# Optimization experiments

Measured on AMD Instinct MI355X. Metric: run time of the kernel, lower is better.

## Reference

```python
import jax, jax.numpy as jnp
import numpy as np

D_MODEL = 1024
NUM_HEADS = 16
ROPE_BASE = 10000.0


def _rope_sincos(T, head_dim, dtype):
    # angles[t, i] = t / base**(2i/head_dim), i in [0, head_dim//2)
    pos = jnp.arange(T, dtype=jnp.float32)[:, None]              # [T, 1]
    inv_freq = 1.0 / (ROPE_BASE ** (jnp.arange(0, head_dim, 2, dtype=jnp.float32) / head_dim))
    angles = pos * inv_freq                                       # [T, half]
    sin = jnp.sin(angles).astype(dtype)[None, :, None, :]         # [1, T, 1, half]
    cos = jnp.cos(angles).astype(dtype)[None, :, None, :]
    return sin, cos


def _apply_rope(x, sin, cos):
    # x: [B, T, H, head_dim]; deinterleave even/odd lanes, rotate, concat halves
    x1, x2 = x[..., ::2], x[..., 1::2]                            # [B, T, H, half] each
    return jnp.concatenate([x1 * cos - x2 * sin, x1 * sin + x2 * cos], axis=-1)


def setup_inputs() -> dict:
    key = jax.random.key(0)
    ks = jax.random.split(key, 5)
    B, T, D = 2, 2048, D_MODEL
    s = 0.02
    return {
        "x": jax.random.normal(ks[0], (B, T, D), dtype=jnp.float32),
        "w_qkv": jax.random.normal(ks[1], (3 * D, D), dtype=jnp.float32) * s,
        "b_qkv": jnp.zeros((3 * D,), dtype=jnp.float32),
        "w_out": jax.random.normal(ks[2], (D, D), dtype=jnp.float32) * s,
        "b_out": jnp.zeros((D,), dtype=jnp.float32),
    }


def reference(x, w_qkv, b_qkv, w_out, b_out):
    B, T, D = x.shape
    H = NUM_HEADS
    hd = D // H
    scale = hd ** -0.5

    qkv = (x @ w_qkv.T + b_qkv).reshape(B, T, 3, H, hd)
    q, k, v = qkv[:, :, 0], qkv[:, :, 1], qkv[:, :, 2]            # [B, T, H, hd]

    sin, cos = _rope_sincos(T, hd, x.dtype)
    q = _apply_rope(q, sin, cos)
    k = _apply_rope(k, sin, cos)

    scores = jnp.einsum("bthd,bshd->bhts", q, k) * scale          # [B, H, T, T]
    weights = jax.nn.softmax(scores, axis=-1)
    out = jnp.einsum("bhts,bshd->bthd", weights, v)               # [B, T, H, hd]
    out = out.reshape(B, T, D)
    return out @ w_out.T + b_out
```

## Files before the change

kernel.cpp:

```cpp
#include <hip/hip_runtime.h>
#include <cstdint>
#include <cstddef>

typedef __attribute__((ext_vector_type(8))) short short8;
typedef __attribute__((ext_vector_type(8))) __bf16 bf16x8;
typedef __attribute__((ext_vector_type(4))) float f32x4;
typedef __attribute__((ext_vector_type(16))) float f32x16;
typedef __attribute__((ext_vector_type(4))) unsigned int uint32x4;

#define LOG2E 1.44269504088896340736f

__device__ __forceinline__ unsigned short f2bf(float f) {
    unsigned int u = __builtin_bit_cast(unsigned int, f);
    u += 0x7fffu + ((u >> 16) & 1u);
    return (unsigned short)(u >> 16);
}

__device__ __forceinline__ f32x4 zero4() {
    f32x4 z; z.x = 0.f; z.y = 0.f; z.z = 0.f; z.w = 0.f; return z;
}
__device__ __forceinline__ f32x16 zero16() {
    f32x16 z;
    #pragma unroll
    for (int i = 0; i < 16; ++i) z[i] = 0.f;
    return z;
}

__device__ __forceinline__ f32x4 mfma16(short8 a, short8 b, f32x4 c) {
    return __builtin_amdgcn_mfma_f32_16x16x32_bf16(
        __builtin_bit_cast(bf16x8, a), __builtin_bit_cast(bf16x8, b), c, 0, 0, 0);
}
__device__ __forceinline__ f32x16 mfma32(short8 a, short8 b, f32x16 c) {
    return __builtin_amdgcn_mfma_f32_32x32x16_bf16(
        __builtin_bit_cast(bf16x8, a), __builtin_bit_cast(bf16x8, b), c, 0, 0, 0);
}

__device__ __forceinline__ unsigned int cvt_pk_bf16(float lo, float hi) {
    unsigned int r;
    asm("v_cvt_pk_bf16_f32 %0, %1, %2" : "=v"(r) : "v"(lo), "v"(hi));
    return r;
}

__device__ __forceinline__ uint2 permswap(unsigned x, unsigned y) {
#if __has_builtin(__builtin_amdgcn_permlane32_swap)
    auto r = __builtin_amdgcn_permlane32_swap(x, y, false, false);
    return make_uint2(r[0], r[1]);
#else
    int lane = threadIdx.x & 63;
    unsigned sy = __shfl_xor(y, 32), sx = __shfl_xor(x, 32);
    return make_uint2((lane < 32) ? x : sy, (lane < 32) ? sx : y);
#endif
}
__device__ __forceinline__ float red_max32(float v) {
    unsigned u = __builtin_bit_cast(unsigned, v);
    uint2 p = permswap(u, u);
    return fmaxf(__builtin_bit_cast(float, p.x), __builtin_bit_cast(float, p.y));
}

__device__ __forceinline__ void gload_lds16(const void* g, void* l, int lane) {
#if __has_builtin(__builtin_amdgcn_global_load_lds)
    __builtin_amdgcn_global_load_lds(
        (const __attribute__((address_space(1))) void*)g,
        (__attribute__((address_space(3))) void*)l, 16, 0, 0);
    (void)lane;
#else
    reinterpret_cast<int4*>(l)[lane] = *reinterpret_cast<const int4*>(g);
#endif
}

__global__ __launch_bounds__(256) void prep_kernel(
    const float* __restrict__ x, const float* __restrict__ wq,
    const float* __restrict__ wo,
    unsigned short* __restrict__ xb, unsigned short* __restrict__ wqb,
    unsigned short* __restrict__ wob, float2* __restrict__ tab) {
    const int S0 = 1048576, S1 = 786432, S2 = 262144;
    int i = blockIdx.x * 256 + threadIdx.x;
    const float* src; unsigned short* dst; int j;
    if (i < S0) { src = x; dst = xb; j = i; }
    else if (i < S0 + S1) { src = wq; dst = wqb; j = i - S0; }
    else if (i < S0 + S1 + S2) { src = wo; dst = wob; j = i - S0 - S1; }
    else {
        int idx = i - (S0 + S1 + S2);
        if (idx < 2048 * 32) {
            int t = idx >> 5, ii = idx & 31;
            float inv_freq = powf(10000.0f, -(float)ii / 32.0f);
            float ang = (float)t * inv_freq;
            tab[idx] = make_float2(cosf(ang), sinf(ang));
        }
        return;
    }
    float4 v = reinterpret_cast<const float4*>(src)[j];
    ushort4 o;
    o.x = f2bf(v.x); o.y = f2bf(v.y); o.z = f2bf(v.z); o.w = f2bf(v.w);
    reinterpret_cast<ushort4*>(dst)[j] = o;
}

template<int BM, int BN, int WMG, int WNG>
__device__ __forceinline__ void gemm_mainloop(
    const unsigned short* __restrict__ A, const unsigned short* __restrict__ B,
    int K, int m0, int n0, char* As, char* Bs,
    f32x4 (&acc)[BM / (WMG * 16)][BN / (WNG * 16)]) {
    constexpr int MT = BM / (WMG * 16), NTT = BN / (WNG * 16);
    constexpr int CA = BM / 64, CB = BN / 64;
    constexpr int ABUF = BM * 128, BBUF = BN * 128;
    int tid = threadIdx.x;
    int wave = tid >> 6, lane = tid & 63;
    int wm = wave / WNG, wn = wave % WNG;
    int g = lane >> 4, c = lane & 15;
    const int NS = K >> 6;

    auto stage = [&](int buf, int k0) {
        #pragma unroll
        for (int i = 0; i < CA; ++i) {
            int call = wave * CA + i;
            int s = call * 64 + lane;
            int row = s >> 3, c8 = s & 7;
            int csw = (c8 ^ (row & 7)) << 3;
            gload_lds16(A + (size_t)(m0 + row) * K + k0 + csw,
                        As + buf * ABUF + call * 1024, lane);
        }
        #pragma unroll
        for (int i = 0; i < CB; ++i) {
            int call = wave * CB + i;
            int s = call * 64 + lane;
            int row = s >> 3, c8 = s & 7;
            int csw = (c8 ^ (row & 7)) << 3;
            gload_lds16(B + (size_t)(n0 + row) * K + k0 + csw,
                        Bs + buf * BBUF + call * 1024, lane);
        }
    };

    stage(0, 0);

    #pragma unroll 1
    for (int t = 0; t < NS; ++t) {
        int cur = t & 1;
        asm volatile("s_waitcnt vmcnt(0)" ::: "memory");
        __builtin_amdgcn_s_barrier();
        __builtin_amdgcn_sched_barrier(0);
        if (t + 1 < NS) stage(cur ^ 1, (t + 1) * 64);

        const char* Ac = As + cur * ABUF;
        const char* Bc = Bs + cur * BBUF;
        #pragma unroll
        for (int kg = 0; kg < 2; ++kg) {
            short8 af[MT], bfr[NTT];
            #pragma unroll
            for (int mt = 0; mt < MT; ++mt) {
                int row = wm * (BM / WMG) + mt * 16 + c;
                af[mt] = *reinterpret_cast<const short8*>(Ac +
                    ((row * 128 + kg * 64 + g * 16) ^ ((row & 7) << 4)));
            }
            #pragma unroll
            for (int nt = 0; nt < NTT; ++nt) {
                int row = wn * (BN / WNG) + nt * 16 + c;
                bfr[nt] = *reinterpret_cast<const short8*>(Bc +
                    ((row * 128 + kg * 64 + g * 16) ^ ((row & 7) << 4)));
            }
            __builtin_amdgcn_s_setprio(1);
            #pragma unroll
            for (int mt = 0; mt < MT; ++mt)
                #pragma unroll
                for (int nt = 0; nt < NTT; ++nt)
                    acc[mt][nt] = mfma16(af[mt], bfr[nt], acc[mt][nt]);
            __builtin_amdgcn_s_setprio(0);
        }
    }
}

__global__ __launch_bounds__(512, 2) void qkv_gemm_kernel(
    const unsigned short* __restrict__ X, const unsigned short* __restrict__ W,
    const float* __restrict__ bias, const float2* __restrict__ tab,
    unsigned short* __restrict__ q, unsigned short* __restrict__ k,
    unsigned short* __restrict__ vt) {
    __shared__ char smem[80 * 1024];
    const int K = 1024;
    const float SCL = 0.125f * LOG2E;
    int flat = blockIdx.x;
    int swzb = (flat & 7) * 64 + (flat >> 3);
    int m0 = (swzb >> 4) * 128, n0 = (swzb & 15) * 192;
    f32x4 acc[2][6];
    #pragma unroll
    for (int i = 0; i < 2; ++i)
        #pragma unroll
        for (int j = 0; j < 6; ++j) acc[i][j] = zero4();

    gemm_mainloop<128, 192, 4, 2>(X, W, K, m0, n0, smem, smem + 32768, acc);

    int tid = threadIdx.x;
    int wave = tid >> 6, lane = tid & 63;
    int wm = wave >> 1, wn = wave & 1;
    int g = lane >> 4, c = lane & 15;
    int mbase = m0 + wm * 32, nbase = n0 + wn * 96;
    #pragma unroll
    for (int mt = 0; mt < 2; ++mt) {
        #pragma unroll
        for (int nt = 0; nt < 6; ++nt) {
            f32x4 a = acc[mt][nt];
            int n = nbase + nt * 16 + c;
            int s = n >> 10;
            int h = (n >> 6) & 15;
            int d = n & 63;
            float bn = bias[n];
            #pragma unroll
            for (int r = 0; r < 4; ++r) {
                int m = mbase + mt * 16 + g * 4 + r;
                int bb = m >> 11, t = m & 2047;
                float val = a[r] + bn;
                float partner = __shfl_xor(val, 1);
                int bh = bb * 16 + h;
                if (s == 2) {
                    vt[((size_t)bh * 64 + d) * 2048 + t] = f2bf(val);
                } else {
                    int i2 = d >> 1;
                    float2 cs = tab[t * 32 + i2];
                    float outv; int dout;
                    if ((d & 1) == 0) { outv = val * cs.x - partner * cs.y; dout = i2; }
                    else              { outv = partner * cs.y + val * cs.x; dout = 32 + i2; }
                    if (s == 0) outv *= SCL;
                    (s == 0 ? q : k)[((size_t)bh * 2048 + t) * 64 + dout] = f2bf(outv);
                }
            }
        }
    }
}

__global__ __launch_bounds__(256, 2) void attn_kernel(
    const unsigned short* __restrict__ Q, const unsigned short* __restrict__ Kin,
    const unsigned short* __restrict__ VT, unsigned short* __restrict__ O) {
    __shared__ int4 smem4[65536 / 16];
    char* smem = (char*)smem4;
    const int T = 2048, NT = 16;
    int flat = blockIdx.x + 16 * blockIdx.y;
    int swzb = (flat & 7) * 64 + (flat >> 3);
    int bh = swzb >> 4;
    int qt = swzb & 15;
    int tid = threadIdx.x, wave = tid >> 6, lane = tid & 63;
    int lam = lane & 31, hi = lane >> 5;
    int q = qt * 128 + wave * 32 + lam;

    const unsigned short* Qb = Q + ((size_t)bh * T + q) * 64;
    const unsigned short* Kb = Kin + (size_t)bh * T * 64;
    const unsigned short* VTb = VT + (size_t)bh * 64 * T;

    uint32x4 qtmp[4];
    #pragma unroll
    for (int c4 = 0; c4 < 4; ++c4)
        qtmp[c4] = *reinterpret_cast<const uint32x4*>(Qb + c4 * 16 + hi * 8);
    #pragma unroll
    for (int c4 = 0; c4 < 4; ++c4)
        asm volatile("" : "+v"(qtmp[c4]));
    short8 qf[4];
    #pragma unroll
    for (int c4 = 0; c4 < 4; ++c4) qf[c4] = __builtin_bit_cast(short8, qtmp[c4]);

    short8 ones;
    #pragma unroll
    for (int i = 0; i < 8; ++i) ones[i] = (short)0x3F80;

    f32x16 o0 = zero16(), o1 = zero16(), lacc = zero16();
    float m_run = -1e30f;
    int swz = (lam & 7) << 4;

    char* KsB = smem;
    char* VsB = smem + 32768;

    auto stage = [&](int buf, int t) {
        int j0 = t * 128;
        #pragma unroll
        for (int st = 0; st < 2; ++st) {
            #pragma unroll
            for (int i = 0; i < 2; ++i) {
                int call = wave * 2 + i;
                int s = call * 64 + lane;
                int row = s >> 3, c8 = s & 7;
                int csw = (c8 ^ (row & 7)) << 3;
                gload_lds16(Kb + (size_t)(j0 + st * 64 + row) * 64 + csw,
                            KsB + buf * 16384 + st * 8192 + call * 1024, lane);
                gload_lds16(VTb + (size_t)row * T + j0 + st * 64 + csw,
                            VsB + buf * 16384 + st * 8192 + call * 1024, lane);
            }
        }
    };

    stage(0, 0);

    #pragma unroll 1
    for (int t = 0; t < NT; ++t) {
        int cur = t & 1;
        asm volatile("s_waitcnt vmcnt(0)" ::: "memory");
        __builtin_amdgcn_s_barrier();
        __builtin_amdgcn_sched_barrier(0);
        if (t + 1 < NT) stage(cur ^ 1, t + 1);

        const char* Kc = KsB + cur * 16384;
        const char* Vc = VsB + cur * 16384;

        f32x16 s0 = zero16(), s1 = zero16(), s2 = zero16(), s3 = zero16();
        __builtin_amdgcn_s_setprio(1);
        #pragma unroll
        for (int c4 = 0; c4 < 4; ++c4) {
            int col = c4 * 32 + hi * 16;
            short8 kf;
            kf = *reinterpret_cast<const short8*>(Kc + ((lam * 128 + col) ^ swz));
            s0 = mfma32(kf, qf[c4], s0);
            kf = *reinterpret_cast<const short8*>(Kc + (((lam + 32) * 128 + col) ^ swz));
            s1 = mfma32(kf, qf[c4], s1);
            kf = *reinterpret_cast<const short8*>(Kc + 8192 + ((lam * 128 + col) ^ swz));
            s2 = mfma32(kf, qf[c4], s2);
            kf = *reinterpret_cast<const short8*>(Kc + 8192 + (((lam + 32) * 128 + col) ^ swz));
            s3 = mfma32(kf, qf[c4], s3);
        }
        __builtin_amdgcn_s_setprio(0);

        short8 vf[8];
        #pragma unroll
        for (int jt = 0; jt < 4; ++jt) {
            int col = jt * 32 + hi * 16;
            vf[jt * 2]     = *reinterpret_cast<const short8*>(Vc + ((lam * 128 + col) ^ swz));
            vf[jt * 2 + 1] = *reinterpret_cast<const short8*>(Vc + (((lam + 32) * 128 + col) ^ swz));
        }

        float mx[16];
        #pragma unroll
        for (int r = 0; r < 16; ++r)
            mx[r] = fmaxf(fmaxf(s0[r], s1[r]), fmaxf(s2[r], s3[r]));
        float tm = mx[0];
        #pragma unroll
        for (int r = 1; r < 16; ++r) tm = fmaxf(tm, mx[r]);
        float tmax = red_max32(tm);
        if (__any(tmax - m_run > 8.0f)) {
            float mnew = fmaxf(m_run, tmax);
            float alpha = exp2f(m_run - mnew);
            m_run = mnew;
            #pragma unroll
            for (int r = 0; r < 16; ++r) {
                o0[r] *= alpha; o1[r] *= alpha; lacc[r] *= alpha;
            }
        }
        float p0[16], p1[16], p2[16], p3[16];
        #pragma unroll
        for (int r = 0; r < 16; ++r) p0[r] = exp2f(s0[r] - m_run);
        #pragma unroll
        for (int r = 0; r < 16; ++r) p1[r] = exp2f(s1[r] - m_run);
        #pragma unroll
        for (int r = 0; r < 16; ++r) p2[r] = exp2f(s2[r] - m_run);
        #pragma unroll
        for (int r = 0; r < 16; ++r) p3[r] = exp2f(s3[r] - m_run);

        short8 pa[8];
        {
            const float* ps[4] = { p0, p1, p2, p3 };
            #pragma unroll
            for (int blk = 0; blk < 4; ++blk) {
                const float* p = ps[blk];
                #pragma unroll
                for (int jt = 0; jt < 2; ++jt) {
                    unsigned a0 = cvt_pk_bf16(p[jt * 8 + 0], p[jt * 8 + 1]);
                    unsigned a1 = cvt_pk_bf16(p[jt * 8 + 2], p[jt * 8 + 3]);
                    unsigned b0 = cvt_pk_bf16(p[jt * 8 + 4], p[jt * 8 + 5]);
                    unsigned b1 = cvt_pk_bf16(p[jt * 8 + 6], p[jt * 8 + 7]);
                    uint2 pr0 = permswap(a0, b0);
                    uint2 pr1 = permswap(a1, b1);
                    uint4 w;
                    w.x = pr0.x;
                    w.y = pr1.x;
                    w.z = pr0.y;
                    w.w = pr1.y;
                    pa[blk * 2 + jt] = __builtin_bit_cast(short8, w);
                }
            }
        }

        __builtin_amdgcn_s_setprio(1);
        #pragma unroll
        for (int jt = 0; jt < 4; ++jt) {
            o0 = mfma32(vf[jt * 2], pa[jt], o0);
            o1 = mfma32(vf[jt * 2 + 1], pa[jt], o1);
            lacc = mfma32(ones, pa[jt], lacc);
        }
        #pragma unroll
        for (int jt = 0; jt < 4; ++jt) {
            int col = jt * 32 + hi * 16;
            short8 vg0 = *reinterpret_cast<const short8*>(Vc + 8192 + ((lam * 128 + col) ^ swz));
            o0 = mfma32(vg0, pa[4 + jt], o0);
            short8 vg1 = *reinterpret_cast<const short8*>(Vc + 8192 + (((lam + 32) * 128 + col) ^ swz));
            o1 = mfma32(vg1, pa[4 + jt], o1);
            lacc = mfma32(ones, pa[4 + jt], lacc);
        }
        __builtin_amdgcn_s_setprio(0);
    }

    float l_run = lacc[0];

    float rinv = 1.0f / l_run;
    int b_ = bh >> 4, h_ = bh & 15;
    unsigned short* Orow = O + ((size_t)(b_ * 2048) + q) * 1024 + h_ * 64;
    #pragma unroll
    for (int rq = 0; rq < 4; ++rq) {
        ushort4 w0, w1;
        w0.x = f2bf(o0[rq * 4 + 0] * rinv);
        w0.y = f2bf(o0[rq * 4 + 1] * rinv);
        w0.z = f2bf(o0[rq * 4 + 2] * rinv);
        w0.w = f2bf(o0[rq * 4 + 3] * rinv);
        w1.x = f2bf(o1[rq * 4 + 0] * rinv);
        w1.y = f2bf(o1[rq * 4 + 1] * rinv);
        w1.z = f2bf(o1[rq * 4 + 2] * rinv);
        w1.w = f2bf(o1[rq * 4 + 3] * rinv);
        int d0 = rq * 8 + hi * 4;
        *reinterpret_cast<ushort4*>(Orow + d0) = w0;
        *reinterpret_cast<ushort4*>(Orow + 32 + d0) = w1;
    }
}

__global__ __launch_bounds__(512, 2) void out_gemm_kernel(
    const unsigned short* __restrict__ Aattn, const unsigned short* __restrict__ W,
    const float* __restrict__ bias, float* __restrict__ out) {
    __shared__ char smem[48 * 1024];
    const int K = 1024, N = 1024;
    int flat = blockIdx.x;
    int swzb = (flat & 7) * 64 + (flat >> 3);
    int m0 = (swzb & 63) * 64, n0 = (swzb >> 6) * 128;
    f32x4 acc[2][2];
    #pragma unroll
    for (int i = 0; i < 2; ++i)
        #pragma unroll
        for (int j = 0; j < 2; ++j) acc[i][j] = zero4();

    gemm_mainloop<64, 128, 2, 4>(Aattn, W, K, m0, n0, smem, smem + 16384, acc);

    int tid = threadIdx.x;
    int wave = tid >> 6, lane = tid & 63;
    int wm = wave >> 2, wn = wave & 3;
    int g = lane >> 4, c = lane & 15;
    int mbase = m0 + wm * 32, nbase = n0 + wn * 32;
    #pragma unroll
    for (int mt = 0; mt < 2; ++mt)
        #pragma unroll
        for (int nt = 0; nt < 2; ++nt) {
            int n = nbase + nt * 16 + c;
            float bn = bias[n];
            #pragma unroll
            for (int r = 0; r < 4; ++r) {
                int m = mbase + mt * 16 + g * 4 + r;
                out[(size_t)m * N + n] = acc[mt][nt][r] + bn;
            }
        }
}

extern "C" void kernel_launch(void* const* d_in, const int* in_sizes, int n_in,
                              void* d_out, int out_size, void* d_ws, size_t ws_size,
                              hipStream_t stream) {
    (void)in_sizes; (void)n_in; (void)out_size; (void)ws_size;
    const float* x     = (const float*)d_in[0];
    const float* w_qkv = (const float*)d_in[1];
    const float* b_qkv = (const float*)d_in[2];
    const float* w_out = (const float*)d_in[3];
    const float* b_out = (const float*)d_in[4];
    float* out = (float*)d_out;

    const int B = 2, T = 2048, D = 1024;
    const int M = B * T;
    const size_t MB = 1024 * 1024;
    (void)D; (void)M;

    char* ws = (char*)d_ws;
    unsigned short* xb    = (unsigned short*)(ws);
    unsigned short* wqkvb = (unsigned short*)(ws + 8 * MB);
    unsigned short* woutb = (unsigned short*)(ws + 14 * MB);
    unsigned short* qb    = (unsigned short*)(ws + 16 * MB);
    unsigned short* kb    = (unsigned short*)(ws + 24 * MB);
    unsigned short* vtb   = (unsigned short*)(ws + 32 * MB);
    unsigned short* attnb = (unsigned short*)(ws + 40 * MB);
    float2* tab           = (float2*)(ws + 48 * MB);

    prep_kernel<<<dim3((2097152 + 65536) / 256), dim3(256), 0, stream>>>(
        x, w_qkv, w_out, xb, wqkvb, woutb, tab);
    qkv_gemm_kernel<<<dim3(512), dim3(512), 0, stream>>>(xb, wqkvb, b_qkv, tab, qb, kb, vtb);
    attn_kernel<<<dim3(T / 128, B * 16), dim3(256), 0, stream>>>(qb, kb, vtb, attnb);
    out_gemm_kernel<<<dim3(512), dim3(512), 0, stream>>>(attnb, woutb, b_out, out);
}
```

Before: 138.8 us.

## Single-buffer K tile and replace ones-MFMA row sum to raise occupancy

The attention kernel now double-buffers only V and keeps a single K buffer, reloaded after QK^T finishes behind an extra barrier. This cuts LDS use from 64KB to 48KB so launch bounds can request 3 blocks per CU. The row-sum accumulator that used extra MFMAs against a ones vector is replaced by a VALU sum plus a cross-half permlane reduction, which frees 16 accumulator registers and a third of the PV MFMAs. In exchange, the K load for the next tile has less time to hide behind compute, there is a second barrier per iteration, and the sums are taken from fp32 probabilities rather than bf16-rounded ones.

```diff
diff --git a/kernel.cpp b/kernel.cpp
--- a/kernel.cpp
+++ b/kernel.cpp
@@ -55,6 +55,11 @@
     unsigned u = __builtin_bit_cast(unsigned, v);
     uint2 p = permswap(u, u);
     return fmaxf(__builtin_bit_cast(float, p.x), __builtin_bit_cast(float, p.y));
+}
+__device__ __forceinline__ float red_add32(float v) {
+    unsigned u = __builtin_bit_cast(unsigned, v);
+    uint2 p = permswap(u, u);
+    return __builtin_bit_cast(float, p.x) + __builtin_bit_cast(float, p.y);
 }
 
 __device__ __forceinline__ void gload_lds16(const void* g, void* l, int lane) {
@@ -225,10 +230,10 @@
     }
 }
 
-__global__ __launch_bounds__(256, 2) void attn_kernel(
+__global__ __launch_bounds__(256, 3) void attn_kernel(
     const unsigned short* __restrict__ Q, const unsigned short* __restrict__ Kin,
     const unsigned short* __restrict__ VT, unsigned short* __restrict__ O) {
-    __shared__ int4 smem4[65536 / 16];
+    __shared__ int4 smem4[49152 / 16];
     char* smem = (char*)smem4;
     const int T = 2048, NT = 16;
     int flat = blockIdx.x + 16 * blockIdx.y;
@@ -254,18 +259,29 @@
     #pragma unroll
     for (int c4 = 0; c4 < 4; ++c4) qf[c4] = __builtin_bit_cast(short8, qtmp[c4]);
 
-    short8 ones;
-    #pragma unroll
-    for (int i = 0; i < 8; ++i) ones[i] = (short)0x3F80;
-
-    f32x16 o0 = zero16(), o1 = zero16(), lacc = zero16();
-    float m_run = -1e30f;
+    f32x16 o0 = zero16(), o1 = zero16();
+    float m_run = -1e30f, l_run = 0.0f;
     int swz = (lam & 7) << 4;
 
-    char* KsB = smem;
-    char* VsB = smem + 32768;
-
-    auto stage = [&](int buf, int t) {
+    char* VsB = smem;
+    char* Ks  = smem + 32768;
+
+    auto stageV = [&](int buf, int t) {
+        int j0 = t * 128;
+        #pragma unroll
+        for (int st = 0; st < 2; ++st) {
+            #pragma unroll
+            for (int i = 0; i < 2; ++i) {
+                int call = wave * 2 + i;
+                int s = call * 64 + lane;
+                int row = s >> 3, c8 = s & 7;
+                int csw = (c8 ^ (row & 7)) << 3;
+                gload_lds16(VTb + (size_t)row * T + j0 + st * 64 + csw,
+                            VsB + buf * 16384 + st * 8192 + call * 1024, lane);
+            }
+        }
+    };
+    auto stageK = [&](int t) {
         int j0 = t * 128;
         #pragma unroll
         for (int st = 0; st < 2; ++st) {
@@ -276,14 +292,13 @@
                 int row = s >> 3, c8 = s & 7;
                 int csw = (c8 ^ (row & 7)) << 3;
                 gload_lds16(Kb + (size_t)(j0 + st * 64 + row) * 64 + csw,
-                            KsB + buf * 16384 + st * 8192 + call * 1024, lane);
-                gload_lds16(VTb + (size_t)row * T + j0 + st * 64 + csw,
-                            VsB + buf * 16384 + st * 8192 + call * 1024, lane);
+                            Ks + st * 8192 + call * 1024, lane);
             }
         }
     };
 
-    stage(0, 0);
+    stageV(0, 0);
+    stageK(0);
 
     #pragma unroll 1
     for (int t = 0; t < NT; ++t) {
@@ -291,9 +306,8 @@
         asm volatile("s_waitcnt vmcnt(0)" ::: "memory");
         __builtin_amdgcn_s_barrier();
         __builtin_amdgcn_sched_barrier(0);
-        if (t + 1 < NT) stage(cur ^ 1, t + 1);
-
-        const char* Kc = KsB + cur * 16384;
+        if (t + 1 < NT) stageV(cur ^ 1, t + 1);
+
         const char* Vc = VsB + cur * 16384;
 
         f32x16 s0 = zero16(), s1 = zero16(), s2 = zero16(), s3 = zero16();
@@ -302,16 +316,21 @@
         for (int c4 = 0; c4 < 4; ++c4) {
             int col = c4 * 32 + hi * 16;
             short8 kf;
-            kf = *reinterpret_cast<const short8*>(Kc + ((lam * 128 + col) ^ swz));
+            kf = *reinterpret_cast<const short8*>(Ks + ((lam * 128 + col) ^ swz));
             s0 = mfma32(kf, qf[c4], s0);
-            kf = *reinterpret_cast<const short8*>(Kc + (((lam + 32) * 128 + col) ^ swz));
+            kf = *reinterpret_cast<const short8*>(Ks + (((lam + 32) * 128 + col) ^ swz));
             s1 = mfma32(kf, qf[c4], s1);
-            kf = *reinterpret_cast<const short8*>(Kc + 8192 + ((lam * 128 + col) ^ swz));
+            kf = *reinterpret_cast<const short8*>(Ks + 8192 + ((lam * 128 + col) ^ swz));
             s2 = mfma32(kf, qf[c4], s2);
-            kf = *reinterpret_cast<const short8*>(Kc + 8192 + (((lam + 32) * 128 + col) ^ swz));
+            kf = *reinterpret_cast<const short8*>(Ks + 8192 + (((lam + 32) * 128 + col) ^ swz));
             s3 = mfma32(kf, qf[c4], s3);
         }
         __builtin_amdgcn_s_setprio(0);
+
+        asm volatile("s_waitcnt lgkmcnt(0)" ::: "memory");
+        __builtin_amdgcn_s_barrier();
+        __builtin_amdgcn_sched_barrier(0);
+        if (t + 1 < NT) stageK(t + 1);
 
         short8 vf[8];
         #pragma unroll
@@ -333,10 +352,9 @@
             float mnew = fmaxf(m_run, tmax);
             float alpha = exp2f(m_run - mnew);
             m_run = mnew;
-            #pragma unroll
-            for (int r = 0; r < 16; ++r) {
-                o0[r] *= alpha; o1[r] *= alpha; lacc[r] *= alpha;
-            }
+            l_run *= alpha;
+            #pragma unroll
+            for (int r = 0; r < 16; ++r) { o0[r] *= alpha; o1[r] *= alpha; }
         }
         float p0[16], p1[16], p2[16], p3[16];
         #pragma unroll
@@ -347,6 +365,15 @@
         for (int r = 0; r < 16; ++r) p2[r] = exp2f(s2[r] - m_run);
         #pragma unroll
         for (int r = 0; r < 16; ++r) p3[r] = exp2f(s3[r] - m_run);
+
+        float sm[16];
+        #pragma unroll
+        for (int r = 0; r < 16; ++r) sm[r] = (p0[r] + p1[r]) + (p2[r] + p3[r]);
+        #pragma unroll
+        for (int st = 8; st > 0; st >>= 1)
+            #pragma unroll
+            for (int r = 0; r < st; ++r) sm[r] += sm[r + st];
+        l_run += red_add32(sm[0]);
 
         short8 pa[8];
         {
@@ -377,7 +404,6 @@
         for (int jt = 0; jt < 4; ++jt) {
             o0 = mfma32(vf[jt * 2], pa[jt], o0);
             o1 = mfma32(vf[jt * 2 + 1], pa[jt], o1);
-            lacc = mfma32(ones, pa[jt], lacc);
         }
         #pragma unroll
         for (int jt = 0; jt < 4; ++jt) {
@@ -386,12 +412,9 @@
             o0 = mfma32(vg0, pa[4 + jt], o0);
             short8 vg1 = *reinterpret_cast<const short8*>(Vc + 8192 + (((lam + 32) * 128 + col) ^ swz));
             o1 = mfma32(vg1, pa[4 + jt], o1);
-            lacc = mfma32(ones, pa[4 + jt], lacc);
         }
         __builtin_amdgcn_s_setprio(0);
     }
-
-    float l_run = lacc[0];
 
     float rinv = 1.0f / l_run;
     int b_ = bh >> 4, h_ = bh & 15;
```

After: 164.1 us. +18.2%, slower.
